# Performance work log

Measured on AMD Instinct MI355X. Metric: run time of the kernel, lower is better.

## Reference

```python
import jax, jax.numpy as jnp
import numpy as np

D = 2048
H = 16
HD = D // H


def setup_inputs() -> dict:
    key = jax.random.key(0)
    k1, k2, k3 = jax.random.split(key, 3)
    x = jax.random.normal(k1, (2, 2048, D), dtype=jnp.float32)
    # torch Linear(d, 3d, bias=False): y = x @ W.T; store transposed weight [D, 3D]
    Wqkv = jax.random.normal(k2, (D, 3 * D), dtype=jnp.float32) * (D ** -0.5)
    Wo = jax.random.normal(k3, (D, D), dtype=jnp.float32) * (D ** -0.5)
    return {"x": x, "Wqkv": Wqkv, "Wo": Wo}


def reference(x, Wqkv, Wo):
    B, S, _ = x.shape
    qkv = (x @ Wqkv).reshape(B, S, 3, H, HD)
    q = qkv[:, :, 0].transpose(0, 2, 1, 3)  # [B,H,S,HD]
    k = qkv[:, :, 1].transpose(0, 2, 1, 3)
    v = qkv[:, :, 2].transpose(0, 2, 1, 3)
    scores = jnp.einsum("bhqd,bhkd->bhqk", q, k) * (HD ** -0.5)
    causal = jnp.tril(jnp.ones((S, S), dtype=bool))  # keep lower triangle
    scores = jnp.where(causal, scores, jnp.float32(-1e9))
    a = jax.nn.softmax(scores, axis=-1)
    o = jnp.einsum("bhqk,bhkd->bhqd", a, v)
    o = o.transpose(0, 2, 1, 3).reshape(B, S, H * HD)
    return o @ Wo
```

## Files before the change

kernel.cpp:

```cpp
#include <hip/hip_runtime.h>
#include <hip/hip_bf16.h>
#include <cstdint>

typedef __bf16 bf16;
typedef __bf16 bf16x8 __attribute__((ext_vector_type(8)));
typedef __bf16 bf16x4 __attribute__((ext_vector_type(4)));
typedef float floatx4 __attribute__((ext_vector_type(4)));

#define MFMA16(a, b, c) __builtin_amdgcn_mfma_f32_16x16x32_bf16(a, b, c, 0, 0, 0)

__device__ __forceinline__ void gload_lds16(const void* g, void* l) {
    __builtin_amdgcn_global_load_lds(
        (const __attribute__((address_space(1))) void*)g,
        (__attribute__((address_space(3))) void*)l, 16, 0, 0);
}

__global__ void downcast_kernel(const float* __restrict__ in, bf16* __restrict__ out,
                                size_t n) {
    const size_t i = ((size_t)blockIdx.x * blockDim.x + threadIdx.x) * 4;
    if (i >= n) return;
    const float4 v = *(const float4*)(in + i);
    bf16x4 o = {(bf16)v.x, (bf16)v.y, (bf16)v.z, (bf16)v.w};
    *(bf16x4*)(out + i) = o;
}

__global__ void transpose_kernel(const float* __restrict__ in, bf16* __restrict__ out,
                                 int R, int C) {
    __shared__ float tile[32][33];
    const int c0 = blockIdx.x * 32, r0 = blockIdx.y * 32;
    const int tx = threadIdx.x & 31, ty = threadIdx.x >> 5;
    for (int i = 0; i < 32; i += 8)
        tile[ty + i][tx] = in[(size_t)(r0 + ty + i) * C + (c0 + tx)];
    __syncthreads();
    for (int i = 0; i < 32; i += 8)
        out[(size_t)(c0 + ty + i) * R + (r0 + tx)] = (bf16)tile[tx][ty + i];
}

template <int MODE>
__global__ __launch_bounds__(256) void gemm_bt_kernel(
    const bf16* __restrict__ A, const bf16* __restrict__ BT,
    int M, int N, int K,
    bf16* __restrict__ qt, bf16* __restrict__ kt, bf16* __restrict__ vt,
    float* __restrict__ Cout) {
    __shared__ alignas(16) bf16 As[128 * 64];
    __shared__ alignas(16) bf16 Bs[128 * 64];

    const int tid = threadIdx.x;
    const int wave = tid >> 6, lane = tid & 63;
    const int quad = lane >> 4, r16 = lane & 15;
    const int m0 = blockIdx.y * 128, n0 = blockIdx.x * 128;
    const int wm = (wave >> 1) * 64, wn = (wave & 1) * 64;

    int srow[4], soff[4];
#pragma unroll
    for (int j = 0; j < 4; ++j) {
        const int c = tid + j * 256;
        srow[j] = c >> 3;
        soff[j] = ((c & 7) ^ (srow[j] & 7)) * 8;
    }

    floatx4 acc[4][4] = {};

    for (int k0 = 0; k0 < K; k0 += 64) {
        __syncthreads();
#pragma unroll
        for (int j = 0; j < 4; ++j) {
            const int c = tid + j * 256;
            gload_lds16(A + (size_t)(m0 + srow[j]) * K + k0 + soff[j], As + c * 8);
            gload_lds16(BT + (size_t)(n0 + srow[j]) * K + k0 + soff[j], Bs + c * 8);
        }
        __syncthreads();

#pragma unroll
        for (int kc = 0; kc < 2; ++kc) {
            bf16x8 a[4], b[4];
#pragma unroll
            for (int i = 0; i < 4; ++i) {
                const int row = wm + i * 16 + r16;
                const int sp = (4 * kc + quad) ^ (row & 7);
                a[i] = *(const bf16x8*)(As + row * 64 + sp * 8);
            }
#pragma unroll
            for (int j = 0; j < 4; ++j) {
                const int row = wn + j * 16 + r16;
                const int sp = (4 * kc + quad) ^ (row & 7);
                b[j] = *(const bf16x8*)(Bs + row * 64 + sp * 8);
            }
#pragma unroll
            for (int i = 0; i < 4; ++i)
#pragma unroll
                for (int j = 0; j < 4; ++j)
                    acc[i][j] = MFMA16(a[i], b[j], acc[i][j]);
        }
    }

    if (MODE == 0) {
        const int t = n0 >> 11;
        const float qscale = 0.08838834764831845f;
#pragma unroll
        for (int i = 0; i < 4; ++i) {
            const int mbase = m0 + wm + i * 16 + quad * 4;
            const int b_ = mbase >> 11;
            const int s = mbase & 2047;
#pragma unroll
            for (int j = 0; j < 4; ++j) {
                const int n = n0 + wn + j * 16 + r16;
                const int h = (n >> 7) & 15, hd = n & 127;
                const int bh = b_ * 16 + h;
                if (t == 0) {
#pragma unroll
                    for (int r = 0; r < 4; ++r)
                        qt[(size_t)(bh * 2048 + s + r) * 128 + hd] =
                            (bf16)(acc[i][j][r] * qscale);
                } else if (t == 1) {
#pragma unroll
                    for (int r = 0; r < 4; ++r)
                        kt[(size_t)(bh * 2048 + s + r) * 128 + hd] = (bf16)acc[i][j][r];
                } else {
                    bf16x4 pv = {(bf16)acc[i][j][0], (bf16)acc[i][j][1],
                                 (bf16)acc[i][j][2], (bf16)acc[i][j][3]};
                    *(bf16x4*)(vt + (size_t)(bh * 128 + hd) * 2048 + s) = pv;
                }
            }
        }
    } else {
#pragma unroll
        for (int i = 0; i < 4; ++i) {
            const int mbase = m0 + wm + i * 16 + quad * 4;
#pragma unroll
            for (int j = 0; j < 4; ++j) {
                const int n = n0 + wn + j * 16 + r16;
#pragma unroll
                for (int r = 0; r < 4; ++r)
                    Cout[(size_t)(mbase + r) * N + n] = acc[i][j][r];
            }
        }
    }
}

__global__ __launch_bounds__(256) void attn_kernel(
    const bf16* __restrict__ qt, const bf16* __restrict__ kt,
    const bf16* __restrict__ vt, bf16* __restrict__ o) {
    __shared__ alignas(16) bf16 Ks[64 * 128];
    __shared__ alignas(16) bf16 Vts[128 * 64];
    __shared__ alignas(16) bf16 Ps[4][16 * 72];

    const int tid = threadIdx.x;
    const int wave = tid >> 6, lane = tid & 63;
    const int quad = lane >> 4, r16 = lane & 15;
    const int pair = blockIdx.x, bh = blockIdx.y;
    const int b_ = bh >> 4, h = bh & 15;

    for (int half = 0; half < 2; ++half) {
        const int t = half == 0 ? pair : 31 - pair;
        const int q0 = t * 64;

        bf16x8 aq[4];
        {
            const bf16* qbase = qt + (((size_t)bh * 2048 + q0 + wave * 16 + r16) << 7);
#pragma unroll
            for (int kc = 0; kc < 4; ++kc)
                aq[kc] = *(const bf16x8*)(qbase + kc * 32 + quad * 8);
        }

        floatx4 oacc[8] = {};
        float lsum[4] = {0.f, 0.f, 0.f, 0.f};

        for (int it = 0; it <= t; ++it) {
            const int k0 = it * 64;
            __syncthreads();
#pragma unroll
            for (int j = 0; j < 4; ++j) {
                const int c = tid + j * 256;
                const int row = c >> 4, sp = c & 15, s = sp ^ (row & 15);
                gload_lds16(kt + (((size_t)bh * 2048 + k0 + row) << 7) + s * 8,
                            Ks + c * 8);
            }
#pragma unroll
            for (int j = 0; j < 4; ++j) {
                const int c = tid + j * 256;
                const int row = c >> 3, sp = c & 7, s = sp ^ (row & 7);
                gload_lds16(vt + ((size_t)bh * 128 + row) * 2048 + k0 + s * 8,
                            Vts + c * 8);
            }
            __syncthreads();

            floatx4 sacc[4] = {};
#pragma unroll
            for (int nt = 0; nt < 4; ++nt) {
                const int row = nt * 16 + r16;
#pragma unroll
                for (int kc = 0; kc < 4; ++kc) {
                    const int sp = (4 * kc + quad) ^ r16;
                    bf16x8 bk = *(const bf16x8*)(Ks + row * 128 + sp * 8);
                    sacc[nt] = MFMA16(aq[kc], bk, sacc[nt]);
                }
            }

            const int qrowC = q0 + wave * 16 + quad * 4;
            float p[4][4];
            if (it == t) {
#pragma unroll
                for (int nt = 0; nt < 4; ++nt)
#pragma unroll
                    for (int r = 0; r < 4; ++r) {
                        const bool ok = (k0 + nt * 16 + r16) <= (qrowC + r);
                        const float e = ok ? __expf(sacc[nt][r]) : 0.f;
                        p[nt][r] = e;
                        lsum[r] += e;
                    }
            } else {
#pragma unroll
                for (int nt = 0; nt < 4; ++nt)
#pragma unroll
                    for (int r = 0; r < 4; ++r) {
                        const float e = __expf(sacc[nt][r]);
                        p[nt][r] = e;
                        lsum[r] += e;
                    }
            }

#pragma unroll
            for (int nt = 0; nt < 4; ++nt)
#pragma unroll
                for (int r = 0; r < 4; ++r)
                    Ps[wave][(quad * 4 + r) * 72 + nt * 16 + r16] = (bf16)p[nt][r];

#pragma unroll
            for (int kblk = 0; kblk < 2; ++kblk) {
                bf16x8 ap = *(const bf16x8*)(&Ps[wave][r16 * 72 + kblk * 32 + quad * 8]);
#pragma unroll
                for (int nt2 = 0; nt2 < 8; ++nt2) {
                    const int row = nt2 * 16 + r16;
                    const int sp = (4 * kblk + quad) ^ (row & 7);
                    bf16x8 bv = *(const bf16x8*)(Vts + row * 64 + sp * 8);
                    oacc[nt2] = MFMA16(ap, bv, oacc[nt2]);
                }
            }
        }

#pragma unroll
        for (int r = 0; r < 4; ++r) {
            float s = lsum[r];
#pragma unroll
            for (int off = 1; off < 16; off <<= 1) s += __shfl_xor(s, off);
            lsum[r] = s;
        }

#pragma unroll
        for (int r = 0; r < 4; ++r) {
            const int qq = q0 + wave * 16 + quad * 4 + r;
            const float inv = 1.0f / lsum[r];
            bf16* orow = o + (size_t)(b_ * 2048 + qq) * 2048 + h * 128;
#pragma unroll
            for (int nt2 = 0; nt2 < 8; ++nt2)
                orow[nt2 * 16 + r16] = (bf16)(oacc[nt2][r] * inv);
        }
    }
}

extern "C" void kernel_launch(void* const* d_in, const int* in_sizes, int n_in,
                              void* d_out, int out_size, void* d_ws, size_t ws_size,
                              hipStream_t stream) {
    const float* x    = (const float*)d_in[0];
    const float* Wqkv = (const float*)d_in[1];
    const float* Wo   = (const float*)d_in[2];
    float* out        = (float*)d_out;

    char* ws = (char*)d_ws;
    bf16* xb    = (bf16*)ws; ws += (size_t)4096 * 2048 * 2;
    bf16* WqkvT = (bf16*)ws; ws += (size_t)6144 * 2048 * 2;
    bf16* WoT   = (bf16*)ws; ws += (size_t)2048 * 2048 * 2;
    bf16* qt    = (bf16*)ws; ws += (size_t)32 * 2048 * 128 * 2;
    bf16* kt    = (bf16*)ws; ws += (size_t)32 * 2048 * 128 * 2;
    bf16* vt    = (bf16*)ws; ws += (size_t)32 * 128 * 2048 * 2;
    bf16* ob    = (bf16*)ws; ws += (size_t)4096 * 2048 * 2;

    downcast_kernel<<<8192, 256, 0, stream>>>(x, xb, (size_t)4096 * 2048);
    transpose_kernel<<<dim3(192, 64), 256, 0, stream>>>(Wqkv, WqkvT, 2048, 6144);
    transpose_kernel<<<dim3(64, 64), 256, 0, stream>>>(Wo, WoT, 2048, 2048);

    gemm_bt_kernel<0><<<dim3(48, 32), 256, 0, stream>>>(
        xb, WqkvT, 4096, 6144, 2048, qt, kt, vt, nullptr);

    attn_kernel<<<dim3(16, 32), 256, 0, stream>>>(qt, kt, vt, ob);

    gemm_bt_kernel<1><<<dim3(16, 32), 256, 0, stream>>>(
        ob, WoT, 4096, 2048, 2048, nullptr, nullptr, nullptr, out);
}
```

Before: 375.1 us.

## Enlarge attention query tile to 128 rows with two M-subtiles per wave

The attention kernel now gives each block one 128-row query tile, with each wave owning 32 rows as two 16-row MFMA subtiles. This replaces the earlier scheme where a block handled a balanced pair of 64-row tiles. Each K/V tile loaded into shared memory now feeds twice as many MFMAs, which cuts global-to-LDS traffic and barriers per unit of work. Blocks are ordered longest-first to soften causal load imbalance. In exchange, each wave holds more accumulator registers, which may lower occupancy, and the per-block workload varies more than under the pairing scheme.

```diff
diff --git a/kernel.cpp b/kernel.cpp
--- a/kernel.cpp
+++ b/kernel.cpp
@@ -143,120 +143,119 @@
     const bf16* __restrict__ vt, bf16* __restrict__ o) {
     __shared__ alignas(16) bf16 Ks[64 * 128];
     __shared__ alignas(16) bf16 Vts[128 * 64];
-    __shared__ alignas(16) bf16 Ps[4][16 * 72];
+    __shared__ alignas(16) bf16 Ps[4][32 * 72];
 
     const int tid = threadIdx.x;
     const int wave = tid >> 6, lane = tid & 63;
     const int quad = lane >> 4, r16 = lane & 15;
-    const int pair = blockIdx.x, bh = blockIdx.y;
+    const int t = 15 - blockIdx.x, bh = blockIdx.y;
     const int b_ = bh >> 4, h = bh & 15;
-
-    for (int half = 0; half < 2; ++half) {
-        const int t = half == 0 ? pair : 31 - pair;
-        const int q0 = t * 64;
-
-        bf16x8 aq[4];
-        {
-            const bf16* qbase = qt + (((size_t)bh * 2048 + q0 + wave * 16 + r16) << 7);
-#pragma unroll
-            for (int kc = 0; kc < 4; ++kc)
-                aq[kc] = *(const bf16x8*)(qbase + kc * 32 + quad * 8);
-        }
-
-        floatx4 oacc[8] = {};
-        float lsum[4] = {0.f, 0.f, 0.f, 0.f};
-
-        for (int it = 0; it <= t; ++it) {
-            const int k0 = it * 64;
-            __syncthreads();
-#pragma unroll
-            for (int j = 0; j < 4; ++j) {
-                const int c = tid + j * 256;
-                const int row = c >> 4, sp = c & 15, s = sp ^ (row & 15);
-                gload_lds16(kt + (((size_t)bh * 2048 + k0 + row) << 7) + s * 8,
-                            Ks + c * 8);
-            }
-#pragma unroll
-            for (int j = 0; j < 4; ++j) {
-                const int c = tid + j * 256;
-                const int row = c >> 3, sp = c & 7, s = sp ^ (row & 7);
-                gload_lds16(vt + ((size_t)bh * 128 + row) * 2048 + k0 + s * 8,
-                            Vts + c * 8);
-            }
-            __syncthreads();
-
-            floatx4 sacc[4] = {};
-#pragma unroll
-            for (int nt = 0; nt < 4; ++nt) {
-                const int row = nt * 16 + r16;
-#pragma unroll
-                for (int kc = 0; kc < 4; ++kc) {
-                    const int sp = (4 * kc + quad) ^ r16;
-                    bf16x8 bk = *(const bf16x8*)(Ks + row * 128 + sp * 8);
-                    sacc[nt] = MFMA16(aq[kc], bk, sacc[nt]);
-                }
-            }
-
-            const int qrowC = q0 + wave * 16 + quad * 4;
-            float p[4][4];
-            if (it == t) {
+    const int q0 = t * 128;
+    const int w0 = q0 + wave * 32;
+
+    bf16x8 aq[2][4];
+#pragma unroll
+    for (int mi = 0; mi < 2; ++mi) {
+        const bf16* qbase = qt + (((size_t)bh * 2048 + w0 + mi * 16 + r16) << 7);
+#pragma unroll
+        for (int kc = 0; kc < 4; ++kc)
+            aq[mi][kc] = *(const bf16x8*)(qbase + kc * 32 + quad * 8);
+    }
+
+    floatx4 oacc[2][8] = {};
+    float lsum[2][4] = {};
+
+    const int niter = 2 * t + 2;
+    for (int it = 0; it < niter; ++it) {
+        const int k0 = it * 64;
+        __syncthreads();
+#pragma unroll
+        for (int j = 0; j < 4; ++j) {
+            const int c = tid + j * 256;
+            const int row = c >> 4, sp = c & 15, s = sp ^ (row & 15);
+            gload_lds16(kt + (((size_t)bh * 2048 + k0 + row) << 7) + s * 8,
+                        Ks + c * 8);
+        }
+#pragma unroll
+        for (int j = 0; j < 4; ++j) {
+            const int c = tid + j * 256;
+            const int row = c >> 3, sp = c & 7, s = sp ^ (row & 7);
+            gload_lds16(vt + ((size_t)bh * 128 + row) * 2048 + k0 + s * 8,
+                        Vts + c * 8);
+        }
+        __syncthreads();
+
+        floatx4 sacc[2][4] = {};
+#pragma unroll
+        for (int nt = 0; nt < 4; ++nt) {
+            const int row = nt * 16 + r16;
+#pragma unroll
+            for (int kc = 0; kc < 4; ++kc) {
+                const int sp = (4 * kc + quad) ^ r16;
+                bf16x8 bk = *(const bf16x8*)(Ks + row * 128 + sp * 8);
+                sacc[0][nt] = MFMA16(aq[0][kc], bk, sacc[0][nt]);
+                sacc[1][nt] = MFMA16(aq[1][kc], bk, sacc[1][nt]);
+            }
+        }
+
+        const bool need_mask = (k0 + 63) > w0;
+#pragma unroll
+        for (int mi = 0; mi < 2; ++mi) {
+            const int qrowC = w0 + mi * 16 + quad * 4;
+            if (need_mask) {
 #pragma unroll
                 for (int nt = 0; nt < 4; ++nt)
 #pragma unroll
                     for (int r = 0; r < 4; ++r) {
                         const bool ok = (k0 + nt * 16 + r16) <= (qrowC + r);
-                        const float e = ok ? __expf(sacc[nt][r]) : 0.f;
-                        p[nt][r] = e;
-                        lsum[r] += e;
+                        const float e = ok ? __expf(sacc[mi][nt][r]) : 0.f;
+                        lsum[mi][r] += e;
+                        Ps[wave][(mi * 16 + quad * 4 + r) * 72 + nt * 16 + r16] =
+                            (bf16)e;
                     }
             } else {
 #pragma unroll
                 for (int nt = 0; nt < 4; ++nt)
 #pragma unroll
                     for (int r = 0; r < 4; ++r) {
-                        const float e = __expf(sacc[nt][r]);
-                        p[nt][r] = e;
-                        lsum[r] += e;
+                        const float e = __expf(sacc[mi][nt][r]);
+                        lsum[mi][r] += e;
+                        Ps[wave][(mi * 16 + quad * 4 + r) * 72 + nt * 16 + r16] =
+                            (bf16)e;
                     }
             }
-
-#pragma unroll
-            for (int nt = 0; nt < 4; ++nt)
-#pragma unroll
-                for (int r = 0; r < 4; ++r)
-                    Ps[wave][(quad * 4 + r) * 72 + nt * 16 + r16] = (bf16)p[nt][r];
-
-#pragma unroll
-            for (int kblk = 0; kblk < 2; ++kblk) {
-                bf16x8 ap = *(const bf16x8*)(&Ps[wave][r16 * 72 + kblk * 32 + quad * 8]);
-#pragma unroll
-                for (int nt2 = 0; nt2 < 8; ++nt2) {
-                    const int row = nt2 * 16 + r16;
-                    const int sp = (4 * kblk + quad) ^ (row & 7);
-                    bf16x8 bv = *(const bf16x8*)(Vts + row * 64 + sp * 8);
-                    oacc[nt2] = MFMA16(ap, bv, oacc[nt2]);
-                }
-            }
-        }
-
+        }
+
+#pragma unroll
+        for (int kblk = 0; kblk < 2; ++kblk) {
+            bf16x8 ap0 = *(const bf16x8*)(&Ps[wave][r16 * 72 + kblk * 32 + quad * 8]);
+            bf16x8 ap1 =
+                *(const bf16x8*)(&Ps[wave][(16 + r16) * 72 + kblk * 32 + quad * 8]);
+#pragma unroll
+            for (int nt2 = 0; nt2 < 8; ++nt2) {
+                const int row = nt2 * 16 + r16;
+                const int sp = (4 * kblk + quad) ^ (row & 7);
+                bf16x8 bv = *(const bf16x8*)(Vts + row * 64 + sp * 8);
+                oacc[0][nt2] = MFMA16(ap0, bv, oacc[0][nt2]);
+                oacc[1][nt2] = MFMA16(ap1, bv, oacc[1][nt2]);
+            }
+        }
+    }
+
+#pragma unroll
+    for (int mi = 0; mi < 2; ++mi)
 #pragma unroll
         for (int r = 0; r < 4; ++r) {
-            float s = lsum[r];
+            float s = lsum[mi][r];
 #pragma unroll
             for (int off = 1; off < 16; off <<= 1) s += __shfl_xor(s, off);
-            lsum[r] = s;
-        }
-
-#pragma unroll
-        for (int r = 0; r < 4; ++r) {
-            const int qq = q0 + wave * 16 + quad * 4 + r;
-            const float inv = 1.0f / lsum[r];
+            const float inv = 1.0f / s;
+            const int qq = w0 + mi * 16 + quad * 4 + r;
             bf16* orow = o + (size_t)(b_ * 2048 + qq) * 2048 + h * 128;
 #pragma unroll
             for (int nt2 = 0; nt2 < 8; ++nt2)
-                orow[nt2 * 16 + r16] = (bf16)(oacc[nt2][r] * inv);
-        }
-    }
+                orow[nt2 * 16 + r16] = (bf16)(oacc[mi][nt2][r] * inv);
+        }
 }
 
 extern "C" void kernel_launch(void* const* d_in, const int* in_sizes, int n_in,
```

Result: slower. 385.2 us (+2.7%).
